# Kernel tuning notes

Measured on AMD Instinct MI355X. Metric: run time of the kernel, lower is better.

The kernel has to match this reference:

```python
import jax, jax.numpy as jnp
import numpy as np

B, S, HID = 2, 2048, 2048
H, KV, D = 16, 8, 128          # query heads, kv heads, head dim
NREP = H // KV
EPS = 1e-6
THETA = 1000000.0
SCALE = 1.0 / np.sqrt(D)


def setup_inputs() -> dict:
    key = jax.random.key(0)
    ks = jax.random.split(key, 5)
    x = jax.random.normal(ks[0], (B, S, HID), jnp.float32)
    std = 0.02
    Wq = jax.random.normal(ks[1], (HID, H * D), jnp.float32) * std
    Wk = jax.random.normal(ks[2], (HID, KV * D), jnp.float32) * std
    Wv = jax.random.normal(ks[3], (HID, KV * D), jnp.float32) * std
    Wo = jax.random.normal(ks[4], (H * D, HID), jnp.float32) * std
    q_norm_w = jnp.ones((D,), jnp.float32)
    k_norm_w = jnp.ones((D,), jnp.float32)
    # standard RoPE cos/sin table: [S, D]
    inv_freq = 1.0 / (THETA ** (jnp.arange(0, D, 2, dtype=jnp.float32) / D))
    freqs = jnp.arange(S, dtype=jnp.float32)[:, None] * inv_freq[None, :]
    emb = jnp.concatenate([freqs, freqs], axis=-1)
    return {"x": x, "Wq": Wq, "Wk": Wk, "Wv": Wv, "Wo": Wo,
            "q_norm_w": q_norm_w, "k_norm_w": k_norm_w,
            "cos": jnp.cos(emb), "sin": jnp.sin(emb)}


def _rmsnorm(x, w, eps=EPS):
    var = jnp.mean(jnp.square(x), axis=-1, keepdims=True)
    return w * (x * jax.lax.rsqrt(var + eps))


def _rotate_half(x):
    x1, x2 = jnp.split(x, 2, axis=-1)
    return jnp.concatenate([-x2, x1], axis=-1)


def _rope(t, cos, sin):
    # t: [B, h, S, D]; cos/sin: [S, D]
    return t * cos[None, None] + _rotate_half(t) * sin[None, None]


def reference(x, Wq, Wk, Wv, Wo, q_norm_w, k_norm_w, cos, sin):
    q = (x @ Wq).reshape(B, S, H, D)
    k = (x @ Wk).reshape(B, S, KV, D)
    v = (x @ Wv).reshape(B, S, KV, D)
    q = _rmsnorm(q, q_norm_w).transpose(0, 2, 1, 3)   # [B, H, S, D]
    k = _rmsnorm(k, k_norm_w).transpose(0, 2, 1, 3)   # [B, KV, S, D]
    v = v.transpose(0, 2, 1, 3)                       # [B, KV, S, D]
    q = _rope(q, cos, sin)
    k = _rope(k, cos, sin)
    # GQA without materializing repeated K/V: group q heads per kv head
    qg = q.reshape(B, KV, NREP, S, D)
    scores = jnp.einsum('bgrsd,bgtd->bgrst', qg, k) * SCALE  # [B,KV,NREP,S,S]
    causal = jnp.tril(jnp.ones((S, S), dtype=bool))
    scores = jnp.where(causal, scores, jnp.finfo(scores.dtype).min)
    p = jax.nn.softmax(scores, axis=-1)
    out = jnp.einsum('bgrst,bgtd->bgrsd', p, v).reshape(B, H, S, D)
    out = out.transpose(0, 2, 1, 3).reshape(B, S, H * D)
    return out @ Wo
```

## Files before the change

### kernel.cpp

```cpp
#include <hip/hip_runtime.h>

typedef unsigned short u16;
typedef __bf16 bf16x8 __attribute__((ext_vector_type(8)));
typedef float f32x4 __attribute__((ext_vector_type(4)));

#define Bn 2
#define Sn 2048
#define HIDn 2048
#define Hn 16
#define KVn 8
#define Dn 128
#define SCALEf 0.08838834764831845f

__device__ __forceinline__ float b2f(u16 v) {
  return __builtin_bit_cast(float, (unsigned)v << 16);
}
__device__ __forceinline__ u16 f2b(float f) {
  unsigned u = __builtin_bit_cast(unsigned, f);
  u += 0x7fffu + ((u >> 16) & 1u);
  return (u16)(u >> 16);
}
__device__ __forceinline__ bool is_bf16(const void* det) {
  return *(const unsigned*)det == 0x3F803F80u;
}
__device__ __forceinline__ float ldx(const void* p, long i, bool isbf) {
  return isbf ? b2f(((const u16*)p)[i]) : ((const float*)p)[i];
}
__device__ __forceinline__ void gl_lds16(const u16* g, u16* l) {
  __builtin_amdgcn_global_load_lds(
      (unsigned int __attribute__((address_space(1)))*)g,
      (unsigned int __attribute__((address_space(3)))*)l, 16, 0, 0);
}

template <int CTRL>
__device__ __forceinline__ float dpp_mov(float x) {
  return __builtin_bit_cast(
      float, __builtin_amdgcn_update_dpp(0, __builtin_bit_cast(int, x), CTRL,
                                         0xF, 0xF, true));
}
__device__ __forceinline__ float red16_max(float x) {
  x = fmaxf(x, dpp_mov<0xB1>(x));
  x = fmaxf(x, dpp_mov<0x4E>(x));
  x = fmaxf(x, dpp_mov<0x141>(x));
  x = fmaxf(x, dpp_mov<0x140>(x));
  return x;
}
__device__ __forceinline__ float red16_sum(float x) {
  x += dpp_mov<0xB1>(x);
  x += dpp_mov<0x4E>(x);
  x += dpp_mov<0x141>(x);
  x += dpp_mov<0x140>(x);
  return x;
}

__global__ __launch_bounds__(256) void convert_x(
    const void* __restrict__ in, u16* __restrict__ out, const void* __restrict__ det) {
  bool isbf = is_bf16(det);
  long i = ((long)blockIdx.x * 256 + threadIdx.x) * 4;
  if (isbf) {
    *(ushort4*)(out + i) = *(const ushort4*)((const u16*)in + i);
  } else {
    float4 f = *(const float4*)((const float*)in + i);
    out[i] = f2b(f.x); out[i + 1] = f2b(f.y); out[i + 2] = f2b(f.z); out[i + 3] = f2b(f.w);
  }
}

__global__ __launch_bounds__(256) void transpose_any(
    const void* __restrict__ vin, u16* __restrict__ out, const void* __restrict__ det,
    int irs, int ors, long ib0, long ob0, int nb1, long ib1, long ob1) {
  __shared__ u16 tile[64][65];
  bool isbf = det ? is_bf16(det) : true;
  int bz = blockIdx.z;
  long ibase = (long)(bz / nb1) * ib0 + (long)(bz % nb1) * ib1;
  u16* op = out + (long)(bz / nb1) * ob0 + (long)(bz % nb1) * ob1;
  long r0 = (long)blockIdx.y * 64, c0 = (long)blockIdx.x * 64;
  int t = threadIdx.x;
  int tr = t >> 3, tc = (t & 7) * 8;
#pragma unroll
  for (int p = 0; p < 2; ++p) {
    int r = p * 32 + tr;
    long src = ibase + (r0 + r) * irs + c0 + tc;
    if (isbf) {
      const u16* ip = (const u16*)vin;
#pragma unroll
      for (int j = 0; j < 8; ++j) tile[r][tc + j] = ip[src + j];
    } else {
      const float* ip = (const float*)vin;
#pragma unroll
      for (int j = 0; j < 8; ++j) tile[r][tc + j] = f2b(ip[src + j]);
    }
  }
  __syncthreads();
#pragma unroll
  for (int p = 0; p < 2; ++p) {
    int r = p * 32 + tr;
    u16* dst = op + (c0 + r) * ors + r0 + tc;
#pragma unroll
    for (int j = 0; j < 8; ++j) dst[j] = tile[tc + j][r];
  }
}

__global__ __launch_bounds__(256) void gemm_bt(
    const u16* __restrict__ A, const u16* __restrict__ Bt, u16* __restrict__ C,
    float* __restrict__ Cf, const void* __restrict__ det, int N, int K) {
  __shared__ alignas(16) u16 As[128 * 64];
  __shared__ alignas(16) u16 Bs[128 * 64];
  int t = threadIdx.x;
  int wave = t >> 6, lane = t & 63, quad = lane >> 4, l15 = lane & 15;
  long bm = (long)blockIdx.y * 128, bn = (long)blockIdx.x * 128;
  int wm = (wave >> 1) * 64, wn = (wave & 1) * 64;
  f32x4 acc[4][4] = {};
  int sg = ((t & 7) ^ ((t >> 3) & 7)) * 8;
  const u16* Ab = A + (bm + (t >> 3)) * K + sg;
  const u16* Bb = Bt + (bn + (t >> 3)) * K + sg;
  for (int k0 = 0; k0 < K; k0 += 64) {
    __syncthreads();
#pragma unroll
    for (int p = 0; p < 4; ++p) {
      gl_lds16(Ab + (long)(p * 32) * K + k0, As + p * 2048 + t * 8);
      gl_lds16(Bb + (long)(p * 32) * K + k0, Bs + p * 2048 + t * 8);
    }
    __syncthreads();
#pragma unroll
    for (int kt = 0; kt < 2; ++kt) {
      int fg = ((kt * 4 + quad) ^ (l15 & 7)) * 8;
      bf16x8 a[4], b[4];
#pragma unroll
      for (int i = 0; i < 4; ++i)
        a[i] = *(const bf16x8*)(As + (wm + i * 16 + l15) * 64 + fg);
#pragma unroll
      for (int j = 0; j < 4; ++j)
        b[j] = *(const bf16x8*)(Bs + (wn + j * 16 + l15) * 64 + fg);
#pragma unroll
      for (int i = 0; i < 4; ++i)
#pragma unroll
        for (int j = 0; j < 4; ++j)
          acc[i][j] = __builtin_amdgcn_mfma_f32_16x16x32_bf16(a[i], b[j], acc[i][j], 0, 0, 0);
    }
  }
  bool tofloat = (Cf != nullptr) && !is_bf16(det);
#pragma unroll
  for (int i = 0; i < 4; ++i) {
    long row = bm + wm + i * 16 + quad * 4;
#pragma unroll
    for (int j = 0; j < 4; ++j) {
      long col = bn + wn + j * 16 + l15;
      if (tofloat) {
#pragma unroll
        for (int r = 0; r < 4; ++r) Cf[(row + r) * N + col] = acc[i][j][r];
      } else {
#pragma unroll
        for (int r = 0; r < 4; ++r) C[(row + r) * N + col] = f2b(acc[i][j][r]);
      }
    }
  }
}

__global__ __launch_bounds__(512, 2) void gemm_qkv256(
    const u16* __restrict__ A, const u16* __restrict__ Bt,
    u16* __restrict__ Qout, u16* __restrict__ Kout, u16* __restrict__ Vout,
    const void* __restrict__ qw, const void* __restrict__ kw,
    const void* __restrict__ cosb, const void* __restrict__ sinb, int K) {
  __shared__ alignas(16) u16 As[2][2][8192];
  __shared__ alignas(16) u16 Bs[2][2][8192];
  const int NT = K >> 6;
  bool isbf = is_bf16(qw);
  int t = threadIdx.x;
  int wave = t >> 6, lane = t & 63, quad = lane >> 4, l15 = lane & 15;
  int l7 = l15 & 7;
  int wmi = wave >> 1, wni = wave & 1;
  long bm = (long)blockIdx.y * 256;
  long bn = (long)blockIdx.x * 256;
  int s0 = t, s1 = t + 512;
  int r0 = s0 >> 3, r1 = s1 >> 3;
  int gs0 = (s0 & 7) ^ (r0 & 7), gs1 = (s1 & 7) ^ (r1 & 7);
  const u16* Ab0 = A + bm * K;
  const u16* Ab1 = A + (bm + 128) * K;
  const u16* Bb0 = Bt + bn * K;
  const u16* Bb1 = Bt + (bn + 128) * K;
#define STG(dst, src)                                          \
  gl_lds16((src) + (long)r0 * K + gs0 * 8, (dst) + s0 * 8);    \
  gl_lds16((src) + (long)r1 * K + gs1 * 8, (dst) + s1 * 8);
  int ah = wmi >> 1;
  int arb = (wmi & 1) * 64 + l15;
#define LDA(m, kk) (*(const bf16x8*)(Ah + (arb + (m)*16) * 64 + ((((kk)*4 + quad) ^ l7) * 8)))
#define LDB(n, kk) (*(const bf16x8*)(Bh + ((n)*16 + l15) * 64 + ((((kk)*4 + quad) ^ l7) * 8)))
  f32x4 acc[4][8] = {};
  STG((u16*)As[0][0], Ab0);
  STG((u16*)As[0][1], Ab1);
  STG((u16*)Bs[0][0], Bb0);
  STG((u16*)Bs[0][1], Bb1);
  asm volatile("s_waitcnt vmcnt(0)" ::: "memory");
  __builtin_amdgcn_s_barrier();

  for (int tk = 0; tk < NT; ++tk) {
    const u16* Ah = (const u16*)As[tk & 1][ah];
    const u16* Bh = (const u16*)Bs[tk & 1][wni];
    int nx = (tk + 1) & 1;
    if (tk + 1 < NT) {
      STG((u16*)As[nx][0], Ab0 + (tk + 1) * 64);
      STG((u16*)As[nx][1], Ab1 + (tk + 1) * 64);
      STG((u16*)Bs[nx][0], Bb0 + (tk + 1) * 64);
      STG((u16*)Bs[nx][1], Bb1 + (tk + 1) * 64);
    }
    bf16x8 a0[4], a1[4], b0[8], b1[8];
#pragma unroll
    for (int m = 0; m < 4; ++m) a0[m] = LDA(m, 0);
#pragma unroll
    for (int n = 0; n < 8; ++n) b0[n] = LDB(n, 0);
#pragma unroll
    for (int m = 0; m < 4; ++m) a1[m] = LDA(m, 1);
#pragma unroll
    for (int n = 0; n < 8; ++n) b1[n] = LDB(n, 1);
    __builtin_amdgcn_s_setprio(1);
#pragma unroll
    for (int m = 0; m < 4; ++m)
#pragma unroll
      for (int j = 0; j < 8; ++j)
        acc[m][j] = __builtin_amdgcn_mfma_f32_16x16x32_bf16(a0[m], b0[j], acc[m][j], 0, 0, 0);
#pragma unroll
    for (int m = 0; m < 4; ++m)
#pragma unroll
      for (int j = 0; j < 8; ++j)
        acc[m][j] = __builtin_amdgcn_mfma_f32_16x16x32_bf16(a1[m], b1[j], acc[m][j], 0, 0, 0);
    __builtin_amdgcn_s_setprio(0);
    asm volatile("s_waitcnt vmcnt(0)" ::: "memory");
    __builtin_amdgcn_s_barrier();
  }
#undef STG
#undef LDA
#undef LDB
  int hglob = (int)(bn >> 7) + wni;
  int mrow0 = (int)bm + wmi * 64 + quad * 4;
  if (hglob < Hn + KVn) {
    bool isq = hglob < Hn;
    const void* w = isq ? qw : kw;
    int nh = isq ? Hn : KVn;
    int hh = isq ? hglob : hglob - Hn;
    u16* Ob = isq ? Qout : Kout;
#pragma unroll
    for (int m = 0; m < 4; ++m) {
#pragma unroll
      for (int r = 0; r < 4; ++r) {
        float ss = 0.f;
#pragma unroll
        for (int j = 0; j < 8; ++j) { float v = acc[m][j][r]; ss += v * v; }
        ss = red16_sum(ss);
        float scale = rsqrtf(ss * (1.0f / 128.0f) + 1e-6f);
        int mr = mrow0 + m * 16 + r;
        int b = mr >> 11, s = mr & (Sn - 1);
        u16* dst = Ob + (((long)b * nh + hh) * Sn + s) * Dn;
        long cb = (long)s * Dn;
#pragma unroll
        for (int j = 0; j < 4; ++j) {
          int c1i = j * 16 + l15, c2i = c1i + 64;
          float x1 = acc[m][j][r] * scale * ldx(w, c1i, isbf);
          float x2 = acc[m][j + 4][r] * scale * ldx(w, c2i, isbf);
          float c1 = ldx(cosb, cb + c1i, isbf), s1 = ldx(sinb, cb + c1i, isbf);
          float c2 = ldx(cosb, cb + c2i, isbf), s2 = ldx(sinb, cb + c2i, isbf);
          dst[c1i] = f2b(x1 * c1 - x2 * s1);
          dst[c2i] = f2b(x2 * c2 + x1 * s2);
        }
      }
    }
  } else {
    int kv = hglob - Hn - KVn;
    int bidx = (int)(bm >> 11);
    int srow = ((int)bm & (Sn - 1)) + wmi * 64 + quad * 4;
#pragma unroll
    for (int m = 0; m < 4; ++m) {
      int sb = srow + m * 16;
#pragma unroll
      for (int j = 0; j < 8; ++j) {
        int d = j * 16 + l15;
        ushort4 tmp;
        tmp.x = f2b(acc[m][j][0]);
        tmp.y = f2b(acc[m][j][1]);
        tmp.z = f2b(acc[m][j][2]);
        tmp.w = f2b(acc[m][j][3]);
        *(ushort4*)(Vout + (((long)bidx * KVn + kv) * Dn + d) * Sn + sb) = tmp;
      }
    }
  }
}

__global__ __launch_bounds__(512) void attn_kernel(
    const u16* __restrict__ Qr, const u16* __restrict__ Kr,
    const u16* __restrict__ Vt, u16* __restrict__ Aout) {
  __shared__ alignas(16) u16 Ks[128 * 128];
  __shared__ alignas(16) u16 Vs[128 * 128];
  __shared__ alignas(16) u16 Ps[8][16 * 128];
  int t = threadIdx.x, wave = t >> 6, lane = t & 63, quad = lane >> 4, l15 = lane & 15;
  int bh = blockIdx.y, b = bh >> 4, h = bh & 15, kvh = h >> 1;
  const u16* kbase = Kr + ((long)b * KVn + kvh) * Sn * Dn;
  const u16* vbase = Vt + ((long)b * KVn + kvh) * (long)Dn * Sn;
  int srow = t >> 4;
  int sgr = ((t & 15) ^ (srow & 15)) * 8;
  u16* ps = (u16*)Ps[wave];

  for (int half = 0; half < 2; ++half) {
    int qt = half == 0 ? (int)blockIdx.x : 15 - (int)blockIdx.x;
    int row0 = qt * 128 + wave * 16;
    const u16* qbase = Qr + (((long)b * Hn + h) * Sn + row0) * Dn;
    bf16x8 aq[4];
#pragma unroll
    for (int kt = 0; kt < 4; ++kt)
      aq[kt] = *(const bf16x8*)(qbase + l15 * Dn + kt * 32 + quad * 8);
    f32x4 o[8] = {};
    float mi[4], li[4];
#pragma unroll
    for (int r = 0; r < 4; ++r) { mi[r] = -1e30f; li[r] = 0.f; }
    int kv_end = qt * 128 + 128;
    for (int kv0 = 0; kv0 < kv_end; kv0 += 128) {
      __syncthreads();
      {
        const u16* kg = kbase + ((long)kv0 + srow) * Dn + sgr;
        const u16* vg = vbase + (long)srow * Sn + kv0 + sgr;
#pragma unroll
        for (int p = 0; p < 4; ++p) {
          gl_lds16(kg + (long)(p * 32) * Dn, Ks + p * 4096 + t * 8);
          gl_lds16(vg + (long)(p * 32) * Sn, Vs + p * 4096 + t * 8);
        }
      }
      __syncthreads();
      f32x4 sc[8] = {};
#pragma unroll
      for (int kt = 0; kt < 4; ++kt) {
        bf16x8 bk[8];
#pragma unroll
        for (int n = 0; n < 8; ++n)
          bk[n] = *(const bf16x8*)(Ks + (n * 16 + l15) * 128 + (((kt * 4 + quad) ^ l15) * 8));
#pragma unroll
        for (int n = 0; n < 8; ++n)
          sc[n] = __builtin_amdgcn_mfma_f32_16x16x32_bf16(aq[kt], bk[n], sc[n], 0, 0, 0);
      }
      f32x4 sv[8];
#pragma unroll
      for (int n = 0; n < 8; ++n)
#pragma unroll
        for (int r = 0; r < 4; ++r) sv[n][r] = sc[n][r] * SCALEf;
      if (kv0 + 127 > row0) {
#pragma unroll
        for (int n = 0; n < 8; ++n) {
          int col = kv0 + n * 16 + l15;
#pragma unroll
          for (int r = 0; r < 4; ++r)
            if (col > row0 + quad * 4 + r) sv[n][r] = -1e30f;
        }
      }
      float alpha[4], pr[4][8];
#pragma unroll
      for (int r = 0; r < 4; ++r) {
        float mx = fmaxf(fmaxf(fmaxf(sv[0][r], sv[1][r]), fmaxf(sv[2][r], sv[3][r])),
                         fmaxf(fmaxf(sv[4][r], sv[5][r]), fmaxf(sv[6][r], sv[7][r])));
        mx = red16_max(mx);
        float mnew = fmaxf(mi[r], mx);
        alpha[r] = __expf(mi[r] - mnew);
        mi[r] = mnew;
        float rs = 0.f;
#pragma unroll
        for (int n = 0; n < 8; ++n) {
          float pv = __expf(sv[n][r] - mnew);
          pr[r][n] = pv;
          rs += pv;
        }
        rs = red16_sum(rs);
        li[r] = li[r] * alpha[r] + rs;
      }
#pragma unroll
      for (int n = 0; n < 8; ++n)
#pragma unroll
        for (int r = 0; r < 4; ++r) o[n][r] *= alpha[r];
#pragma unroll
      for (int n = 0; n < 8; ++n)
#pragma unroll
        for (int r = 0; r < 4; ++r) {
          int prow = quad * 4 + r;
          int pg = (n * 2 + (l15 >> 3)) ^ prow;
          ps[prow * 128 + pg * 8 + (l15 & 7)] = f2b(pr[r][n]);
        }
#pragma unroll
      for (int kt2 = 0; kt2 < 4; ++kt2) {
        bf16x8 ap = *(const bf16x8*)(ps + l15 * 128 + (((kt2 * 4 + quad) ^ l15) * 8));
#pragma unroll
        for (int n = 0; n < 8; ++n) {
          bf16x8 bv = *(const bf16x8*)(Vs + (n * 16 + l15) * 128 + (((kt2 * 4 + quad) ^ l15) * 8));
          o[n] = __builtin_amdgcn_mfma_f32_16x16x32_bf16(ap, bv, o[n], 0, 0, 0);
        }
      }
    }
#pragma unroll
    for (int r = 0; r < 4; ++r) {
      long s = row0 + quad * 4 + r;
      float inv = 1.0f / li[r];
      u16* dst = Aout + (((long)b * Sn + s) * Hn + h) * Dn;
#pragma unroll
      for (int n = 0; n < 8; ++n) dst[n * 16 + l15] = f2b(o[n][r] * inv);
    }
  }
}

extern "C" void kernel_launch(void* const* d_in, const int* in_sizes, int n_in,
                              void* d_out, int out_size, void* d_ws, size_t ws_size,
                              hipStream_t stream) {
  (void)in_sizes; (void)n_in; (void)out_size; (void)ws_size;
  const void* x    = d_in[0];
  const void* Wq   = d_in[1];
  const void* Wk   = d_in[2];
  const void* Wv   = d_in[3];
  const void* Wo   = d_in[4];
  const void* qw   = d_in[5];
  const void* kw   = d_in[6];
  const void* cosb = d_in[7];
  const void* sinb = d_in[8];
  u16* ws = (u16*)d_ws;
  u16* dsc = (u16*)d_out;

  u16* Qr = dsc + 0;
  u16* Kr = dsc + 8388608;
  u16* Vt = dsc + 12582912;
  u16* xb = ws + 0;
  u16* WT = ws + 8388608;
  dim3 blk(256);
  convert_x<<<dim3(8192), blk, 0, stream>>>(x, xb, qw);
  transpose_any<<<dim3(32, 32, 1), blk, 0, stream>>>(Wq, WT, qw, 2048, 2048, 0, 0, 1, 0, 0);
  transpose_any<<<dim3(16, 32, 1), blk, 0, stream>>>(Wk, WT + (long)2048 * 2048, qw, 1024, 2048, 0, 0, 1, 0, 0);
  transpose_any<<<dim3(16, 32, 1), blk, 0, stream>>>(Wv, WT + (long)3072 * 2048, qw, 1024, 2048, 0, 0, 1, 0, 0);
  gemm_qkv256<<<dim3(16, 16), dim3(512), 0, stream>>>(xb, WT, Qr, Kr, Vt,
                                                      qw, kw, cosb, sinb, 2048);
  u16* attn = ws + 0;
  attn_kernel<<<dim3(8, 32), dim3(512), 0, stream>>>(Qr, Kr, Vt, attn);
  u16* WoT = ws + 8388608;
  transpose_any<<<dim3(32, 32, 1), blk, 0, stream>>>(Wo, WoT, qw, 2048, 2048, 0, 0, 1, 0, 0);
  gemm_bt<<<dim3(16, 32), blk, 0, stream>>>(attn, WoT, (u16*)d_out, (float*)d_out, qw, 2048, 2048);
}
```

Baseline: 361.8 us.

## Rewrite output projection GEMM with 256x128 tiles and double-buffered LDS prefetch

Replaces the 128x128 single-buffered output GEMM with a 512-thread kernel computing 256x128 tiles. It double-buffers the A and B tiles in LDS so the next K-slice loads overlap the current MFMAs, and uses one barrier per iteration. It also raises wave priority around the MFMA block. This targets load latency and barrier stalls in the Wo projection, at the cost of more LDS per block and only 256 blocks in the grid.

```diff
diff --git a/kernel.cpp b/kernel.cpp
--- a/kernel.cpp
+++ b/kernel.cpp
@@ -100,57 +100,87 @@
   }
 }
 
-__global__ __launch_bounds__(256) void gemm_bt(
+__global__ __launch_bounds__(512, 2) void gemm_out256(
     const u16* __restrict__ A, const u16* __restrict__ Bt, u16* __restrict__ C,
     float* __restrict__ Cf, const void* __restrict__ det, int N, int K) {
-  __shared__ alignas(16) u16 As[128 * 64];
-  __shared__ alignas(16) u16 Bs[128 * 64];
+  __shared__ alignas(16) u16 As[2][2][8192];
+  __shared__ alignas(16) u16 Bs[2][8192];
+  const int NT = K >> 6;
   int t = threadIdx.x;
   int wave = t >> 6, lane = t & 63, quad = lane >> 4, l15 = lane & 15;
-  long bm = (long)blockIdx.y * 128, bn = (long)blockIdx.x * 128;
-  int wm = (wave >> 1) * 64, wn = (wave & 1) * 64;
+  int l7 = l15 & 7;
+  int wmi = wave >> 1, wni = wave & 1;
+  long bm = (long)blockIdx.y * 256;
+  long bn = (long)blockIdx.x * 128;
+  int s0 = t, s1 = t + 512;
+  int r0 = s0 >> 3, r1 = s1 >> 3;
+  int gs0 = (s0 & 7) ^ (r0 & 7), gs1 = (s1 & 7) ^ (r1 & 7);
+  const u16* Ab0 = A + bm * K;
+  const u16* Ab1 = A + (bm + 128) * K;
+  const u16* Bb  = Bt + bn * K;
+#define STG(dst, src)                                          \
+  gl_lds16((src) + (long)r0 * K + gs0 * 8, (dst) + s0 * 8);    \
+  gl_lds16((src) + (long)r1 * K + gs1 * 8, (dst) + s1 * 8);
+  int ah = wmi >> 1;
+  int arb = (wmi & 1) * 64 + l15;
+#define LDA(m, kk) (*(const bf16x8*)(Ah + (arb + (m)*16) * 64 + ((((kk)*4 + quad) ^ l7) * 8)))
+#define LDB(n, kk) (*(const bf16x8*)(Bh + (wni * 64 + (n)*16 + l15) * 64 + ((((kk)*4 + quad) ^ l7) * 8)))
   f32x4 acc[4][4] = {};
-  int sg = ((t & 7) ^ ((t >> 3) & 7)) * 8;
-  const u16* Ab = A + (bm + (t >> 3)) * K + sg;
-  const u16* Bb = Bt + (bn + (t >> 3)) * K + sg;
-  for (int k0 = 0; k0 < K; k0 += 64) {
-    __syncthreads();
-#pragma unroll
-    for (int p = 0; p < 4; ++p) {
-      gl_lds16(Ab + (long)(p * 32) * K + k0, As + p * 2048 + t * 8);
-      gl_lds16(Bb + (long)(p * 32) * K + k0, Bs + p * 2048 + t * 8);
-    }
-    __syncthreads();
-#pragma unroll
-    for (int kt = 0; kt < 2; ++kt) {
-      int fg = ((kt * 4 + quad) ^ (l15 & 7)) * 8;
-      bf16x8 a[4], b[4];
-#pragma unroll
-      for (int i = 0; i < 4; ++i)
-        a[i] = *(const bf16x8*)(As + (wm + i * 16 + l15) * 64 + fg);
+  STG((u16*)As[0][0], Ab0);
+  STG((u16*)As[0][1], Ab1);
+  STG((u16*)Bs[0], Bb);
+  asm volatile("s_waitcnt vmcnt(0)" ::: "memory");
+  __builtin_amdgcn_s_barrier();
+
+  for (int tk = 0; tk < NT; ++tk) {
+    const u16* Ah = (const u16*)As[tk & 1][ah];
+    const u16* Bh = (const u16*)Bs[tk & 1];
+    int nx = (tk + 1) & 1;
+    if (tk + 1 < NT) {
+      STG((u16*)As[nx][0], Ab0 + (tk + 1) * 64);
+      STG((u16*)As[nx][1], Ab1 + (tk + 1) * 64);
+      STG((u16*)Bs[nx], Bb + (tk + 1) * 64);
+    }
+    bf16x8 a0[4], a1[4], b0[4], b1[4];
+#pragma unroll
+    for (int m = 0; m < 4; ++m) a0[m] = LDA(m, 0);
+#pragma unroll
+    for (int n = 0; n < 4; ++n) b0[n] = LDB(n, 0);
+#pragma unroll
+    for (int m = 0; m < 4; ++m) a1[m] = LDA(m, 1);
+#pragma unroll
+    for (int n = 0; n < 4; ++n) b1[n] = LDB(n, 1);
+    __builtin_amdgcn_s_setprio(1);
+#pragma unroll
+    for (int m = 0; m < 4; ++m)
 #pragma unroll
       for (int j = 0; j < 4; ++j)
-        b[j] = *(const bf16x8*)(Bs + (wn + j * 16 + l15) * 64 + fg);
-#pragma unroll
-      for (int i = 0; i < 4; ++i)
-#pragma unroll
-        for (int j = 0; j < 4; ++j)
-          acc[i][j] = __builtin_amdgcn_mfma_f32_16x16x32_bf16(a[i], b[j], acc[i][j], 0, 0, 0);
-    }
-  }
+        acc[m][j] = __builtin_amdgcn_mfma_f32_16x16x32_bf16(a0[m], b0[j], acc[m][j], 0, 0, 0);
+#pragma unroll
+    for (int m = 0; m < 4; ++m)
+#pragma unroll
+      for (int j = 0; j < 4; ++j)
+        acc[m][j] = __builtin_amdgcn_mfma_f32_16x16x32_bf16(a1[m], b1[j], acc[m][j], 0, 0, 0);
+    __builtin_amdgcn_s_setprio(0);
+    asm volatile("s_waitcnt vmcnt(0)" ::: "memory");
+    __builtin_amdgcn_s_barrier();
+  }
+#undef STG
+#undef LDA
+#undef LDB
   bool tofloat = (Cf != nullptr) && !is_bf16(det);
 #pragma unroll
-  for (int i = 0; i < 4; ++i) {
-    long row = bm + wm + i * 16 + quad * 4;
+  for (int m = 0; m < 4; ++m) {
+    long row = bm + wmi * 64 + m * 16 + quad * 4;
 #pragma unroll
     for (int j = 0; j < 4; ++j) {
-      long col = bn + wn + j * 16 + l15;
+      long col = bn + wni * 64 + j * 16 + l15;
       if (tofloat) {
 #pragma unroll
-        for (int r = 0; r < 4; ++r) Cf[(row + r) * N + col] = acc[i][j][r];
+        for (int r = 0; r < 4; ++r) Cf[(row + r) * N + col] = acc[m][j][r];
       } else {
 #pragma unroll
-        for (int r = 0; r < 4; ++r) C[(row + r) * N + col] = f2b(acc[i][j][r]);
+        for (int r = 0; r < 4; ++r) C[(row + r) * N + col] = f2b(acc[m][j][r]);
       }
     }
   }
@@ -432,5 +462,6 @@
   attn_kernel<<<dim3(8, 32), dim3(512), 0, stream>>>(Qr, Kr, Vt, attn);
   u16* WoT = ws + 8388608;
   transpose_any<<<dim3(32, 32, 1), blk, 0, stream>>>(Wo, WoT, qw, 2048, 2048, 0, 0, 1, 0, 0);
-  gemm_bt<<<dim3(16, 32), blk, 0, stream>>>(attn, WoT, (u16*)d_out, (float*)d_out, qw, 2048, 2048);
-}
+  gemm_out256<<<dim3(16, 16), dim3(512), 0, stream>>>(attn, WoT, (u16*)d_out,
+                                                      (float*)d_out, qw, 2048, 2048);
+}
```

Measured after the change: 363.3 us. About the same (+0.4%).
